# Kernel tuning notes

Hardware: AMD Instinct MI355X
Metric: run time of the kernel (lower is better)

The kernel has to match this reference:

```python
import jax, jax.numpy as jnp
from jax import lax
import numpy as np

T, B, I = 512, 64, 1024
L, H = 2, 1024

def setup_inputs() -> dict:
    key = jax.random.key(0)
    k1, k2, k3 = jax.random.split(key, 3)
    scale = 1.0 / np.sqrt(H)
    return {
        "x": jax.random.normal(k1, (T, B, I), dtype=jnp.float32),
        "w_ih": jax.random.normal(k2, (L, 4 * H, I), dtype=jnp.float32) * scale,
        "w_hh": jax.random.normal(k3, (L, 4 * H, H), dtype=jnp.float32) * scale,
        "b_ih": jnp.zeros((L, 4 * H), dtype=jnp.float32),
        "b_hh": jnp.zeros((L, 4 * H), dtype=jnp.float32),
    }

def _lstm_layer(seq, wi, wh, b):
    # seq: [T, B, D]; wi: [4H, D]; wh: [4H, H]; b: [4H]
    Bsz = seq.shape[1]
    Hh = wh.shape[1]
    # precompute input projection for all timesteps (one big GEMM)
    xin = jnp.einsum('tbd,gd->tbg', seq, wi) + b  # [T, B, 4H]
    def step(carry, xt):
        h, c = carry
        gates = xt + h @ wh.T  # [B, 4H]
        i, f, g, o = jnp.split(gates, 4, axis=1)
        c = jax.nn.sigmoid(f) * c + jax.nn.sigmoid(i) * jnp.tanh(g)
        h = jax.nn.sigmoid(o) * jnp.tanh(c)
        return (h, c), h
    h0 = jnp.zeros((Bsz, Hh), seq.dtype)
    c0 = jnp.zeros((Bsz, Hh), seq.dtype)
    (hn, cn), out = lax.scan(step, (h0, c0), xin)
    return out, hn, cn

def reference(x, w_ih, w_hh, b_ih, b_hh):
    seq = x
    h_n, c_n = [], []
    for l in range(w_hh.shape[0]):
        seq, hn, cn = _lstm_layer(seq, w_ih[l], w_hh[l], b_ih[l] + b_hh[l])
        h_n.append(hn)
        c_n.append(cn)
    return seq, jnp.stack(h_n, 0), jnp.stack(c_n, 0)
```

## Files before the change

### kernel.cpp

```cpp
#include <hip/hip_runtime.h>
#include <cstddef>
#include <cstdint>

#define T_LEN   512
#define BATCH   64
#define IN_DIM  1024
#define HID     1024
#define GATES   4096
#define NLAYERS 2
#define TCHUNK  64
#define BH      (BATCH * HID)
#define RBLK    256

typedef __bf16 bf16;
typedef __bf16 bf16x8 __attribute__((ext_vector_type(8)));
typedef float  f32x4  __attribute__((ext_vector_type(4)));

__global__ __launch_bounds__(256) void cvt_bf16(const float* __restrict__ in,
                                                bf16* __restrict__ out, int n4) {
    int i = blockIdx.x * blockDim.x + threadIdx.x;
    if (i >= n4) return;
    float4 v = ((const float4*)in)[i];
    bf16 o[4] = {(bf16)v.x, (bf16)v.y, (bf16)v.z, (bf16)v.w};
    *(uint2*)(out + 4 * (size_t)i) = *(uint2*)o;
}

template <bool AF32>
__global__ __launch_bounds__(256) void gemm_xin(
    const void* __restrict__ Aptr, const bf16* __restrict__ W,
    const float* __restrict__ bih, const float* __restrict__ bhh,
    float* __restrict__ C)
{
    __shared__ bf16 As[128 * 40];
    __shared__ bf16 Bs[128 * 40];

    const int m0 = blockIdx.y * 128;
    const int n0 = blockIdx.x * 128;
    const int tid  = threadIdx.x;
    const int lane = tid & 63;
    const int wv   = tid >> 6;
    const int wm   = (wv & 1) * 64;
    const int wn   = (wv >> 1) * 64;
    const int quad = lane >> 4;
    const int l16  = lane & 15;

    f32x4 acc[4][4] = {};

    for (int k0 = 0; k0 < IN_DIM; k0 += 32) {
        if constexpr (AF32) {
            const float* A = (const float*)Aptr;
            const int row = tid >> 3;
            const int ko  = (tid & 7) * 4;
            #pragma unroll
            for (int p = 0; p < 4; ++p) {
                int r = row + 32 * p;
                float4 v = *(const float4*)(A + (size_t)(m0 + r) * IN_DIM + k0 + ko);
                bf16 o[4] = {(bf16)v.x, (bf16)v.y, (bf16)v.z, (bf16)v.w};
                *(uint2*)&As[r * 40 + ko] = *(uint2*)o;
            }
        } else {
            const bf16* A = (const bf16*)Aptr;
            const int row = tid >> 2;
            const int ko  = (tid & 3) * 8;
            *(uint4*)&As[row * 40 + ko] =
                *(const uint4*)(A + (size_t)(m0 + row) * IN_DIM + k0 + ko);
            *(uint4*)&As[(row + 64) * 40 + ko] =
                *(const uint4*)(A + (size_t)(m0 + row + 64) * IN_DIM + k0 + ko);
        }
        {
            const int row = tid >> 2;
            const int ko  = (tid & 3) * 8;
            *(uint4*)&Bs[row * 40 + ko] =
                *(const uint4*)(W + (size_t)(n0 + row) * IN_DIM + k0 + ko);
            *(uint4*)&Bs[(row + 64) * 40 + ko] =
                *(const uint4*)(W + (size_t)(n0 + row + 64) * IN_DIM + k0 + ko);
        }
        __syncthreads();

        bf16x8 af[4], bfr[4];
        #pragma unroll
        for (int t = 0; t < 4; ++t) {
            af[t]  = *(const bf16x8*)&As[(wm + t * 16 + l16) * 40 + quad * 8];
            bfr[t] = *(const bf16x8*)&Bs[(wn + t * 16 + l16) * 40 + quad * 8];
        }
        #pragma unroll
        for (int mt = 0; mt < 4; ++mt)
            #pragma unroll
            for (int nt = 0; nt < 4; ++nt)
                acc[mt][nt] = __builtin_amdgcn_mfma_f32_16x16x32_bf16(
                    af[mt], bfr[nt], acc[mt][nt], 0, 0, 0);
        __syncthreads();
    }

    #pragma unroll
    for (int nt = 0; nt < 4; ++nt) {
        int col = n0 + wn + nt * 16 + l16;
        float bias = bih[col] + bhh[col];
        #pragma unroll
        for (int mt = 0; mt < 4; ++mt) {
            #pragma unroll
            for (int r = 0; r < 4; ++r) {
                int row = m0 + wm + mt * 16 + quad * 4 + r;
                C[(size_t)row * GATES + col] = acc[mt][nt][r] + bias;
            }
        }
    }
}

__global__ __launch_bounds__(256) void lstm_chunk(
    const bf16*  __restrict__ wh,
    const float* __restrict__ xg,
    float*       __restrict__ cbuf,
    float*       __restrict__ hf32,
    bf16*        __restrict__ hrot,
    bf16*        __restrict__ seq_bf,
    float*       __restrict__ seq_f32,
    unsigned*    __restrict__ bar,
    int t0)
{
    __shared__ bf16  Bs[16 * 1032];
    __shared__ float sg[4 * 272];

    const int bk   = blockIdx.x;
    const int j0   = bk * 4;
    const int tid  = threadIdx.x;
    const int lane = tid & 63;
    const int wv   = tid >> 6;
    const int m0   = wv * 16;
    const int quad = lane >> 4;
    const int l16  = lane & 15;

    unsigned* flags   = bar;
    unsigned* release = bar + 384;

    #pragma unroll
    for (int i = 0; i < 8; ++i) {
        int flat = i * 256 + tid;
        int row  = flat >> 7;
        int k16  = flat & 127;
        int grr  = (row >> 2) * 1024 + j0 + (row & 3);
        *(uint4*)&Bs[row * 1032 + k16 * 8] =
            *(const uint4*)(wh + (size_t)grr * HID + k16 * 8);
    }

    const int cb = m0 + l16;
    const int cu = j0 + quad;
    float c = cbuf[(size_t)cb * HID + cu];

    const int gr = (l16 >> 2) * 1024 + j0 + (l16 & 3);
    const int bb = m0 + quad * 4;

    float xv0 = xg[(size_t)(bb + 0) * GATES + gr];
    float xv1 = xg[(size_t)(bb + 1) * GATES + gr];
    float xv2 = xg[(size_t)(bb + 2) * GATES + gr];
    float xv3 = xg[(size_t)(bb + 3) * GATES + gr];

    __syncthreads();

    const bf16* bbase = &Bs[l16 * 1032 + quad * 8];

    for (int tt = 0; tt < TCHUNK; ++tt) {
        const bf16* hin  = hrot + (size_t)tt * BH;
        bf16*       hout = hrot + (size_t)((tt + 1) & (TCHUNK - 1)) * BH;

        f32x4 acc0 = {xv0, xv1, xv2, xv3};
        f32x4 acc1 = {0.f, 0.f, 0.f, 0.f};
        f32x4 acc2 = {0.f, 0.f, 0.f, 0.f};
        f32x4 acc3 = {0.f, 0.f, 0.f, 0.f};

        const bf16* aptr = hin + (size_t)(m0 + l16) * HID + quad * 8;
        #pragma unroll
        for (int q = 0; q < 8; ++q) {
            const int k0 = q * 32;
            bf16x8 a0 = *(const bf16x8*)(aptr + k0);
            bf16x8 b0 = *(const bf16x8*)(bbase + k0);
            acc0 = __builtin_amdgcn_mfma_f32_16x16x32_bf16(a0, b0, acc0, 0, 0, 0);
            bf16x8 a1 = *(const bf16x8*)(aptr + 256 + k0);
            bf16x8 b1 = *(const bf16x8*)(bbase + 256 + k0);
            acc1 = __builtin_amdgcn_mfma_f32_16x16x32_bf16(a1, b1, acc1, 0, 0, 0);
            bf16x8 a2 = *(const bf16x8*)(aptr + 512 + k0);
            bf16x8 b2 = *(const bf16x8*)(bbase + 512 + k0);
            acc2 = __builtin_amdgcn_mfma_f32_16x16x32_bf16(a2, b2, acc2, 0, 0, 0);
            bf16x8 a3 = *(const bf16x8*)(aptr + 768 + k0);
            bf16x8 b3 = *(const bf16x8*)(bbase + 768 + k0);
            acc3 = __builtin_amdgcn_mfma_f32_16x16x32_bf16(a3, b3, acc3, 0, 0, 0);
        }

        if (tt + 1 < TCHUNK) {
            const float* xn = xg + (size_t)(tt + 1) * BATCH * GATES;
            xv0 = xn[(size_t)(bb + 0) * GATES + gr];
            xv1 = xn[(size_t)(bb + 1) * GATES + gr];
            xv2 = xn[(size_t)(bb + 2) * GATES + gr];
            xv3 = xn[(size_t)(bb + 3) * GATES + gr];
        }

        f32x4 g4 = (acc0 + acc1) + (acc2 + acc3);

        #pragma unroll
        for (int r = 0; r < 4; ++r)
            sg[wv * 272 + (quad * 4 + r) * 17 + l16] = g4[r];
        const float* gp = &sg[wv * 272 + l16 * 17];
        float gi = gp[quad], gf = gp[4 + quad], gg = gp[8 + quad], go = gp[12 + quad];

        float si  = 1.f / (1.f + expf(-gi));
        float sf_ = 1.f / (1.f + expf(-gf));
        float so  = 1.f / (1.f + expf(-go));
        float cv  = sf_ * c + si * tanhf(gg);
        float hv  = so * tanhf(cv);
        c = cv;

        const int t = t0 + tt;
        const size_t idx = (size_t)cb * HID + cu;
        bf16 hb = (bf16)hv;

        float hvn = __shfl_xor(hv, 16);
        if ((quad & 1) == 0) {
            bf16 hbn = (bf16)hvn;
            unsigned pk = (unsigned)__builtin_bit_cast(unsigned short, hb) |
                          ((unsigned)__builtin_bit_cast(unsigned short, hbn) << 16);
            __hip_atomic_store((unsigned*)(hout + idx), pk,
                               __ATOMIC_RELAXED, __HIP_MEMORY_SCOPE_AGENT);
        }
        if (seq_bf)  seq_bf[(size_t)t * BH + idx] = hb;
        if (seq_f32) seq_f32[(size_t)t * BH + idx] = hv;
        if (t == T_LEN - 1) hf32[idx] = hv;

        if (tt != TCHUNK - 1) {
            const unsigned ep = (unsigned)(tt + 1);
            asm volatile("s_waitcnt vmcnt(0)" ::: "memory");
            __syncthreads();
            if (tid == 0)
                __hip_atomic_store(flags + bk, ep,
                                   __ATOMIC_RELAXED, __HIP_MEMORY_SCOPE_AGENT);
            if (bk == 0 && tid < 64) {
                unsigned guard = 0;
                for (;;) {
                    unsigned f0 = __hip_atomic_load(flags + tid,
                                   __ATOMIC_RELAXED, __HIP_MEMORY_SCOPE_AGENT);
                    unsigned f1 = __hip_atomic_load(flags + 64 + tid,
                                   __ATOMIC_RELAXED, __HIP_MEMORY_SCOPE_AGENT);
                    unsigned f2 = __hip_atomic_load(flags + 128 + tid,
                                   __ATOMIC_RELAXED, __HIP_MEMORY_SCOPE_AGENT);
                    unsigned f3 = __hip_atomic_load(flags + 192 + tid,
                                   __ATOMIC_RELAXED, __HIP_MEMORY_SCOPE_AGENT);
                    if (__all(f0 >= ep && f1 >= ep && f2 >= ep && f3 >= ep)) break;
                    __builtin_amdgcn_s_sleep(1);
                    if (++guard > (1u << 16)) break;
                }
                if (tid == 0)
                    __hip_atomic_store(release, ep,
                                       __ATOMIC_RELAXED, __HIP_MEMORY_SCOPE_AGENT);
            }
            if (tid == 0) {
                unsigned guard = 0;
                while (__hip_atomic_load(release, __ATOMIC_RELAXED,
                                         __HIP_MEMORY_SCOPE_AGENT) < ep) {
                    __builtin_amdgcn_s_sleep(1);
                    if (++guard > (1u << 16)) break;
                }
            }
            __syncthreads();
        }
    }

    cbuf[(size_t)cb * HID + cu] = c;
}

extern "C" void kernel_launch(void* const* d_in, const int* in_sizes, int n_in,
                              void* d_out, int out_size, void* d_ws, size_t ws_size,
                              hipStream_t stream) {
    const float* x    = (const float*)d_in[0];
    const float* w_ih = (const float*)d_in[1];
    const float* w_hh = (const float*)d_in[2];
    const float* b_ih = (const float*)d_in[3];
    const float* b_hh = (const float*)d_in[4];
    float* out = (float*)d_out;

    float* xin  = (float*)d_ws;
    float* cbuf = xin + (size_t)TCHUNK * BATCH * GATES;
    float* hf32 = cbuf + (size_t)BATCH * HID;
    bf16* seq1bf = (bf16*)(hf32 + (size_t)BATCH * HID);
    bf16* wibf   = seq1bf + (size_t)T_LEN * BATCH * HID;
    bf16* whbf   = wibf + (size_t)GATES * IN_DIM;
    bf16* hrot   = whbf + (size_t)GATES * HID;
    unsigned* bar = (unsigned*)(hrot + (size_t)TCHUNK * BATCH * HID);

    const size_t seqE = (size_t)T_LEN * BATCH * HID;
    const size_t BHs  = (size_t)BATCH * HID;

    for (int l = 0; l < NLAYERS; ++l) {
        const float* wi = w_ih + (size_t)l * GATES * IN_DIM;
        const float* wh = w_hh + (size_t)l * GATES * HID;
        const float* bi = b_ih + (size_t)l * GATES;
        const float* bh = b_hh + (size_t)l * GATES;

        cvt_bf16<<<(GATES * IN_DIM / 4 + 255) / 256, 256, 0, stream>>>(wi, wibf, GATES * IN_DIM / 4);
        cvt_bf16<<<(GATES * HID / 4 + 255) / 256, 256, 0, stream>>>(wh, whbf, GATES * HID / 4);

        hipMemsetAsync(hrot, 0, BHs * sizeof(bf16), stream);
        hipMemsetAsync(cbuf, 0, BHs * sizeof(float), stream);

        for (int ch = 0; ch < T_LEN / TCHUNK; ++ch) {
            if (l == 0) {
                const float* Ab = x + (size_t)ch * TCHUNK * BATCH * IN_DIM;
                gemm_xin<true><<<dim3(GATES / 128, TCHUNK * BATCH / 128), 256, 0, stream>>>(
                    Ab, wibf, bi, bh, xin);
            } else {
                const bf16* Ab = seq1bf + (size_t)ch * TCHUNK * BATCH * HID;
                gemm_xin<false><<<dim3(GATES / 128, TCHUNK * BATCH / 128), 256, 0, stream>>>(
                    Ab, wibf, bi, bh, xin);
            }
            hipMemsetAsync(bar, 0, 512 * sizeof(unsigned), stream);
            int t0 = ch * TCHUNK;
            const bf16*  whc = whbf;
            const float* xgc = xin;
            bf16*  sb = (l == 0) ? seq1bf : nullptr;
            float* sf = (l == 1) ? out : nullptr;
            void* args[9] = { (void*)&whc, (void*)&xgc, (void*)&cbuf, (void*)&hf32,
                              (void*)&hrot, (void*)&sb, (void*)&sf, (void*)&bar,
                              (void*)&t0 };
            hipLaunchCooperativeKernel((void*)lstm_chunk, dim3(RBLK), dim3(256),
                                       args, 0, stream);
        }
        hipMemcpyAsync(out + seqE + (size_t)l * BHs, hf32, BHs * sizeof(float),
                       hipMemcpyDeviceToDevice, stream);
        hipMemcpyAsync(out + seqE + (size_t)(NLAYERS + l) * BHs, cbuf, BHs * sizeof(float),
                       hipMemcpyDeviceToDevice, stream);
    }
}
```

Before: 8.865 ms.

## Fuse input projection into persistent per-layer LSTM kernel, overlap with barrier wait

```diff
diff --git a/kernel.cpp b/kernel.cpp
--- a/kernel.cpp
+++ b/kernel.cpp
@@ -8,7 +8,6 @@
 #define HID     1024
 #define GATES   4096
 #define NLAYERS 2
-#define TCHUNK  64
 #define BH      (BATCH * HID)
 #define RBLK    256
 
@@ -25,100 +24,20 @@
     *(uint2*)(out + 4 * (size_t)i) = *(uint2*)o;
 }
 
-template <bool AF32>
-__global__ __launch_bounds__(256) void gemm_xin(
-    const void* __restrict__ Aptr, const bf16* __restrict__ W,
-    const float* __restrict__ bih, const float* __restrict__ bhh,
-    float* __restrict__ C)
+__global__ __launch_bounds__(256) void lstm_layer(
+    const bf16*  __restrict__ wi,
+    const bf16*  __restrict__ wh,
+    const float* __restrict__ bih,
+    const float* __restrict__ bhh,
+    const bf16*  __restrict__ xbf,
+    bf16*        __restrict__ hseq,
+    float*       __restrict__ outf,
+    float*       __restrict__ hf32,
+    float*       __restrict__ cbuf,
+    unsigned*    __restrict__ bar)
 {
-    __shared__ bf16 As[128 * 40];
-    __shared__ bf16 Bs[128 * 40];
-
-    const int m0 = blockIdx.y * 128;
-    const int n0 = blockIdx.x * 128;
-    const int tid  = threadIdx.x;
-    const int lane = tid & 63;
-    const int wv   = tid >> 6;
-    const int wm   = (wv & 1) * 64;
-    const int wn   = (wv >> 1) * 64;
-    const int quad = lane >> 4;
-    const int l16  = lane & 15;
-
-    f32x4 acc[4][4] = {};
-
-    for (int k0 = 0; k0 < IN_DIM; k0 += 32) {
-        if constexpr (AF32) {
-            const float* A = (const float*)Aptr;
-            const int row = tid >> 3;
-            const int ko  = (tid & 7) * 4;
-            #pragma unroll
-            for (int p = 0; p < 4; ++p) {
-                int r = row + 32 * p;
-                float4 v = *(const float4*)(A + (size_t)(m0 + r) * IN_DIM + k0 + ko);
-                bf16 o[4] = {(bf16)v.x, (bf16)v.y, (bf16)v.z, (bf16)v.w};
-                *(uint2*)&As[r * 40 + ko] = *(uint2*)o;
-            }
-        } else {
-            const bf16* A = (const bf16*)Aptr;
-            const int row = tid >> 2;
-            const int ko  = (tid & 3) * 8;
-            *(uint4*)&As[row * 40 + ko] =
-                *(const uint4*)(A + (size_t)(m0 + row) * IN_DIM + k0 + ko);
-            *(uint4*)&As[(row + 64) * 40 + ko] =
-                *(const uint4*)(A + (size_t)(m0 + row + 64) * IN_DIM + k0 + ko);
-        }
-        {
-            const int row = tid >> 2;
-            const int ko  = (tid & 3) * 8;
-            *(uint4*)&Bs[row * 40 + ko] =
-                *(const uint4*)(W + (size_t)(n0 + row) * IN_DIM + k0 + ko);
-            *(uint4*)&Bs[(row + 64) * 40 + ko] =
-                *(const uint4*)(W + (size_t)(n0 + row + 64) * IN_DIM + k0 + ko);
-        }
-        __syncthreads();
-
-        bf16x8 af[4], bfr[4];
-        #pragma unroll
-        for (int t = 0; t < 4; ++t) {
-            af[t]  = *(const bf16x8*)&As[(wm + t * 16 + l16) * 40 + quad * 8];
-            bfr[t] = *(const bf16x8*)&Bs[(wn + t * 16 + l16) * 40 + quad * 8];
-        }
-        #pragma unroll
-        for (int mt = 0; mt < 4; ++mt)
-            #pragma unroll
-            for (int nt = 0; nt < 4; ++nt)
-                acc[mt][nt] = __builtin_amdgcn_mfma_f32_16x16x32_bf16(
-                    af[mt], bfr[nt], acc[mt][nt], 0, 0, 0);
-        __syncthreads();
-    }
-
-    #pragma unroll
-    for (int nt = 0; nt < 4; ++nt) {
-        int col = n0 + wn + nt * 16 + l16;
-        float bias = bih[col] + bhh[col];
-        #pragma unroll
-        for (int mt = 0; mt < 4; ++mt) {
-            #pragma unroll
-            for (int r = 0; r < 4; ++r) {
-                int row = m0 + wm + mt * 16 + quad * 4 + r;
-                C[(size_t)row * GATES + col] = acc[mt][nt][r] + bias;
-            }
-        }
-    }
-}
-
-__global__ __launch_bounds__(256) void lstm_chunk(
-    const bf16*  __restrict__ wh,
-    const float* __restrict__ xg,
-    float*       __restrict__ cbuf,
-    float*       __restrict__ hf32,
-    bf16*        __restrict__ hrot,
-    bf16*        __restrict__ seq_bf,
-    float*       __restrict__ seq_f32,
-    unsigned*    __restrict__ bar,
-    int t0)
-{
-    __shared__ bf16  Bs[16 * 1032];
+    __shared__ bf16  Bi[16 * 1032];
+    __shared__ bf16  Bh[16 * 1032];
     __shared__ float sg[4 * 272];
 
     const int bk   = blockIdx.x;
@@ -139,59 +58,72 @@
         int row  = flat >> 7;
         int k16  = flat & 127;
         int grr  = (row >> 2) * 1024 + j0 + (row & 3);
-        *(uint4*)&Bs[row * 1032 + k16 * 8] =
+        *(uint4*)&Bi[row * 1032 + k16 * 8] =
+            *(const uint4*)(wi + (size_t)grr * IN_DIM + k16 * 8);
+        *(uint4*)&Bh[row * 1032 + k16 * 8] =
             *(const uint4*)(wh + (size_t)grr * HID + k16 * 8);
     }
 
     const int cb = m0 + l16;
     const int cu = j0 + quad;
-    float c = cbuf[(size_t)cb * HID + cu];
+    float c = 0.f;
 
     const int gr = (l16 >> 2) * 1024 + j0 + (l16 & 3);
     const int bb = m0 + quad * 4;
-
-    float xv0 = xg[(size_t)(bb + 0) * GATES + gr];
-    float xv1 = xg[(size_t)(bb + 1) * GATES + gr];
-    float xv2 = xg[(size_t)(bb + 2) * GATES + gr];
-    float xv3 = xg[(size_t)(bb + 3) * GATES + gr];
+    const float bias = bih[gr] + bhh[gr];
 
     __syncthreads();
 
-    const bf16* bbase = &Bs[l16 * 1032 + quad * 8];
-
-    for (int tt = 0; tt < TCHUNK; ++tt) {
-        const bf16* hin  = hrot + (size_t)tt * BH;
-        bf16*       hout = hrot + (size_t)((tt + 1) & (TCHUNK - 1)) * BH;
-
-        f32x4 acc0 = {xv0, xv1, xv2, xv3};
-        f32x4 acc1 = {0.f, 0.f, 0.f, 0.f};
-        f32x4 acc2 = {0.f, 0.f, 0.f, 0.f};
-        f32x4 acc3 = {0.f, 0.f, 0.f, 0.f};
-
-        const bf16* aptr = hin + (size_t)(m0 + l16) * HID + quad * 8;
+    const bf16*  bibase = &Bi[l16 * 1032 + quad * 8];
+    const bf16*  bhbase = &Bh[l16 * 1032 + quad * 8];
+    const size_t arow   = (size_t)(m0 + l16) * HID + quad * 8;
+
+    f32x4 acc0, acc1, acc2, acc3;
+    {
+        const bf16* xp = xbf + arow;
+        acc0 = {bias, bias, bias, bias};
+        acc1 = {0.f, 0.f, 0.f, 0.f};
+        acc2 = {0.f, 0.f, 0.f, 0.f};
+        acc3 = {0.f, 0.f, 0.f, 0.f};
         #pragma unroll
         for (int q = 0; q < 8; ++q) {
             const int k0 = q * 32;
-            bf16x8 a0 = *(const bf16x8*)(aptr + k0);
-            bf16x8 b0 = *(const bf16x8*)(bbase + k0);
-            acc0 = __builtin_amdgcn_mfma_f32_16x16x32_bf16(a0, b0, acc0, 0, 0, 0);
-            bf16x8 a1 = *(const bf16x8*)(aptr + 256 + k0);
-            bf16x8 b1 = *(const bf16x8*)(bbase + 256 + k0);
-            acc1 = __builtin_amdgcn_mfma_f32_16x16x32_bf16(a1, b1, acc1, 0, 0, 0);
-            bf16x8 a2 = *(const bf16x8*)(aptr + 512 + k0);
-            bf16x8 b2 = *(const bf16x8*)(bbase + 512 + k0);
-            acc2 = __builtin_amdgcn_mfma_f32_16x16x32_bf16(a2, b2, acc2, 0, 0, 0);
-            bf16x8 a3 = *(const bf16x8*)(aptr + 768 + k0);
-            bf16x8 b3 = *(const bf16x8*)(bbase + 768 + k0);
-            acc3 = __builtin_amdgcn_mfma_f32_16x16x32_bf16(a3, b3, acc3, 0, 0, 0);
-        }
-
-        if (tt + 1 < TCHUNK) {
-            const float* xn = xg + (size_t)(tt + 1) * BATCH * GATES;
-            xv0 = xn[(size_t)(bb + 0) * GATES + gr];
-            xv1 = xn[(size_t)(bb + 1) * GATES + gr];
-            xv2 = xn[(size_t)(bb + 2) * GATES + gr];
-            xv3 = xn[(size_t)(bb + 3) * GATES + gr];
+            acc0 = __builtin_amdgcn_mfma_f32_16x16x32_bf16(
+                *(const bf16x8*)(xp + k0),       *(const bf16x8*)(bibase + k0),       acc0, 0, 0, 0);
+            acc1 = __builtin_amdgcn_mfma_f32_16x16x32_bf16(
+                *(const bf16x8*)(xp + 256 + k0), *(const bf16x8*)(bibase + 256 + k0), acc1, 0, 0, 0);
+            acc2 = __builtin_amdgcn_mfma_f32_16x16x32_bf16(
+                *(const bf16x8*)(xp + 512 + k0), *(const bf16x8*)(bibase + 512 + k0), acc2, 0, 0, 0);
+            acc3 = __builtin_amdgcn_mfma_f32_16x16x32_bf16(
+                *(const bf16x8*)(xp + 768 + k0), *(const bf16x8*)(bibase + 768 + k0), acc3, 0, 0, 0);
+        }
+    }
+
+    for (int tt = 0; tt < T_LEN; ++tt) {
+        if (tt > 0) {
+            const unsigned ep = (unsigned)tt;
+            if (tid == 0) {
+                unsigned guard = 0;
+                while (__hip_atomic_load(release, __ATOMIC_RELAXED,
+                                         __HIP_MEMORY_SCOPE_AGENT) < ep) {
+                    __builtin_amdgcn_s_sleep(1);
+                    if (++guard > (1u << 16)) break;
+                }
+            }
+            __syncthreads();
+            const bf16* hp = hseq + (size_t)(tt - 1) * BH + arow;
+            #pragma unroll
+            for (int q = 0; q < 8; ++q) {
+                const int k0 = q * 32;
+                acc0 = __builtin_amdgcn_mfma_f32_16x16x32_bf16(
+                    *(const bf16x8*)(hp + k0),       *(const bf16x8*)(bhbase + k0),       acc0, 0, 0, 0);
+                acc1 = __builtin_amdgcn_mfma_f32_16x16x32_bf16(
+                    *(const bf16x8*)(hp + 256 + k0), *(const bf16x8*)(bhbase + 256 + k0), acc1, 0, 0, 0);
+                acc2 = __builtin_amdgcn_mfma_f32_16x16x32_bf16(
+                    *(const bf16x8*)(hp + 512 + k0), *(const bf16x8*)(bhbase + 512 + k0), acc2, 0, 0, 0);
+                acc3 = __builtin_amdgcn_mfma_f32_16x16x32_bf16(
+                    *(const bf16x8*)(hp + 768 + k0), *(const bf16x8*)(bhbase + 768 + k0), acc3, 0, 0, 0);
+            }
         }
 
         f32x4 g4 = (acc0 + acc1) + (acc2 + acc3);
@@ -209,29 +141,45 @@
         float hv  = so * tanhf(cv);
         c = cv;
 
-        const int t = t0 + tt;
         const size_t idx = (size_t)cb * HID + cu;
-        bf16 hb = (bf16)hv;
-
         float hvn = __shfl_xor(hv, 16);
         if ((quad & 1) == 0) {
+            bf16 hb  = (bf16)hv;
             bf16 hbn = (bf16)hvn;
             unsigned pk = (unsigned)__builtin_bit_cast(unsigned short, hb) |
                           ((unsigned)__builtin_bit_cast(unsigned short, hbn) << 16);
-            __hip_atomic_store((unsigned*)(hout + idx), pk,
+            __hip_atomic_store((unsigned*)(hseq + (size_t)tt * BH + idx), pk,
                                __ATOMIC_RELAXED, __HIP_MEMORY_SCOPE_AGENT);
         }
-        if (seq_bf)  seq_bf[(size_t)t * BH + idx] = hb;
-        if (seq_f32) seq_f32[(size_t)t * BH + idx] = hv;
-        if (t == T_LEN - 1) hf32[idx] = hv;
-
-        if (tt != TCHUNK - 1) {
+        if (outf) outf[(size_t)tt * BH + idx] = hv;
+        if (tt == T_LEN - 1) hf32[idx] = hv;
+
+        if (tt != T_LEN - 1) {
             const unsigned ep = (unsigned)(tt + 1);
             asm volatile("s_waitcnt vmcnt(0)" ::: "memory");
             __syncthreads();
             if (tid == 0)
                 __hip_atomic_store(flags + bk, ep,
                                    __ATOMIC_RELAXED, __HIP_MEMORY_SCOPE_AGENT);
+
+            const bf16* xp = xbf + (size_t)(tt + 1) * BH + arow;
+            acc0 = {bias, bias, bias, bias};
+            acc1 = {0.f, 0.f, 0.f, 0.f};
+            acc2 = {0.f, 0.f, 0.f, 0.f};
+            acc3 = {0.f, 0.f, 0.f, 0.f};
+            #pragma unroll
+            for (int q = 0; q < 8; ++q) {
+                const int k0 = q * 32;
+                acc0 = __builtin_amdgcn_mfma_f32_16x16x32_bf16(
+                    *(const bf16x8*)(xp + k0),       *(const bf16x8*)(bibase + k0),       acc0, 0, 0, 0);
+                acc1 = __builtin_amdgcn_mfma_f32_16x16x32_bf16(
+                    *(const bf16x8*)(xp + 256 + k0), *(const bf16x8*)(bibase + 256 + k0), acc1, 0, 0, 0);
+                acc2 = __builtin_amdgcn_mfma_f32_16x16x32_bf16(
+                    *(const bf16x8*)(xp + 512 + k0), *(const bf16x8*)(bibase + 512 + k0), acc2, 0, 0, 0);
+                acc3 = __builtin_amdgcn_mfma_f32_16x16x32_bf16(
+                    *(const bf16x8*)(xp + 768 + k0), *(const bf16x8*)(bibase + 768 + k0), acc3, 0, 0, 0);
+            }
+
             if (bk == 0 && tid < 64) {
                 unsigned guard = 0;
                 for (;;) {
@@ -251,15 +199,6 @@
                     __hip_atomic_store(release, ep,
                                        __ATOMIC_RELAXED, __HIP_MEMORY_SCOPE_AGENT);
             }
-            if (tid == 0) {
-                unsigned guard = 0;
-                while (__hip_atomic_load(release, __ATOMIC_RELAXED,
-                                         __HIP_MEMORY_SCOPE_AGENT) < ep) {
-                    __builtin_amdgcn_s_sleep(1);
-                    if (++guard > (1u << 16)) break;
-                }
-            }
-            __syncthreads();
         }
     }
 
@@ -276,17 +215,18 @@
     const float* b_hh = (const float*)d_in[4];
     float* out = (float*)d_out;
 
-    float* xin  = (float*)d_ws;
-    float* cbuf = xin + (size_t)TCHUNK * BATCH * GATES;
+    float* cbuf = (float*)d_ws;
     float* hf32 = cbuf + (size_t)BATCH * HID;
     bf16* seq1bf = (bf16*)(hf32 + (size_t)BATCH * HID);
-    bf16* wibf   = seq1bf + (size_t)T_LEN * BATCH * HID;
+    bf16* xh0    = seq1bf + (size_t)T_LEN * BATCH * HID;
+    bf16* wibf   = xh0 + (size_t)T_LEN * BATCH * HID;
     bf16* whbf   = wibf + (size_t)GATES * IN_DIM;
-    bf16* hrot   = whbf + (size_t)GATES * HID;
-    unsigned* bar = (unsigned*)(hrot + (size_t)TCHUNK * BATCH * HID);
+    unsigned* bar = (unsigned*)(whbf + (size_t)GATES * HID);
 
     const size_t seqE = (size_t)T_LEN * BATCH * HID;
     const size_t BHs  = (size_t)BATCH * HID;
+
+    cvt_bf16<<<(int)(seqE / 4 + 255) / 256, 256, 0, stream>>>(x, xh0, (int)(seqE / 4));
 
     for (int l = 0; l < NLAYERS; ++l) {
         const float* wi = w_ih + (size_t)l * GATES * IN_DIM;
@@ -297,31 +237,21 @@
         cvt_bf16<<<(GATES * IN_DIM / 4 + 255) / 256, 256, 0, stream>>>(wi, wibf, GATES * IN_DIM / 4);
         cvt_bf16<<<(GATES * HID / 4 + 255) / 256, 256, 0, stream>>>(wh, whbf, GATES * HID / 4);
 
-        hipMemsetAsync(hrot, 0, BHs * sizeof(bf16), stream);
-        hipMemsetAsync(cbuf, 0, BHs * sizeof(float), stream);
-
-        for (int ch = 0; ch < T_LEN / TCHUNK; ++ch) {
-            if (l == 0) {
-                const float* Ab = x + (size_t)ch * TCHUNK * BATCH * IN_DIM;
-                gemm_xin<true><<<dim3(GATES / 128, TCHUNK * BATCH / 128), 256, 0, stream>>>(
-                    Ab, wibf, bi, bh, xin);
-            } else {
-                const bf16* Ab = seq1bf + (size_t)ch * TCHUNK * BATCH * HID;
-                gemm_xin<false><<<dim3(GATES / 128, TCHUNK * BATCH / 128), 256, 0, stream>>>(
-                    Ab, wibf, bi, bh, xin);
-            }
-            hipMemsetAsync(bar, 0, 512 * sizeof(unsigned), stream);
-            int t0 = ch * TCHUNK;
-            const bf16*  whc = whbf;
-            const float* xgc = xin;
-            bf16*  sb = (l == 0) ? seq1bf : nullptr;
-            float* sf = (l == 1) ? out : nullptr;
-            void* args[9] = { (void*)&whc, (void*)&xgc, (void*)&cbuf, (void*)&hf32,
-                              (void*)&hrot, (void*)&sb, (void*)&sf, (void*)&bar,
-                              (void*)&t0 };
-            hipLaunchCooperativeKernel((void*)lstm_chunk, dim3(RBLK), dim3(256),
-                                       args, 0, stream);
-        }
+        hipMemsetAsync(bar, 0, 512 * sizeof(unsigned), stream);
+
+        const bf16* xin_l = (l == 0) ? xh0 : seq1bf;
+        bf16*       hseq  = (l == 0) ? seq1bf : xh0;
+        float*      outf  = (l == 1) ? out : nullptr;
+
+        const bf16*  wic = wibf;  const bf16* whc = whbf;
+        const float* bic = bi;    const float* bhc = bh;
+        float* hfc = hf32;  float* cbc = cbuf;  unsigned* barc = bar;
+        void* args[10] = { (void*)&wic, (void*)&whc, (void*)&bic, (void*)&bhc,
+                           (void*)&xin_l, (void*)&hseq, (void*)&outf,
+                           (void*)&hfc, (void*)&cbc, (void*)&barc };
+        hipLaunchCooperativeKernel((void*)lstm_layer, dim3(RBLK), dim3(256),
+                                   args, 0, stream);
+
         hipMemcpyAsync(out + seqE + (size_t)l * BHs, hf32, BHs * sizeof(float),
                        hipMemcpyDeviceToDevice, stream);
         hipMemcpyAsync(out + seqE + (size_t)(NLAYERS + l) * BHs, cbuf, BHs * sizeof(float),
```

Result: slower. 10.15 ms (+14.6%).
